# Kernel tuning notes

Hardware: AMD Instinct MI355X
Metric: run time of the kernel (lower is better)

Reference implementation:

```python
import jax, jax.numpy as jnp
import numpy as np

B, S, D, H = 16, 512, 1024, 16
DH = D // H  # 64


def setup_inputs() -> dict:
    key = jax.random.key(0)
    kx, kq, kk, kv = jax.random.split(key, 4)
    stdv = 1.0 / np.sqrt(DH)  # reset_param uses 1/sqrt(t.size(1)) = 1/sqrt(head_dim)
    x = jax.random.normal(kx, (B, S, D), dtype=jnp.float32)
    Wq = jax.random.uniform(kq, (H, D, DH), dtype=jnp.float32, minval=-stdv, maxval=stdv)
    Wk = jax.random.uniform(kk, (H, D, DH), dtype=jnp.float32, minval=-stdv, maxval=stdv)
    Wv = jax.random.uniform(kv, (H, D, DH), dtype=jnp.float32, minval=-stdv, maxval=stdv)
    return {"x": x, "Wq": Wq, "Wk": Wk, "Wv": Wv}


def reference(x, Wq, Wk, Wv):
    # x: [B, S, D]; Wq/Wk/Wv: [H, D, DH] (stacked per-head params)
    q = jnp.einsum('bsd,hde->bhse', x, Wq)  # [B,H,S,DH]
    k = jnp.einsum('bsd,hde->bhse', x, Wk)
    v = jnp.einsum('bsd,hde->bhse', x, Wv)
    # NOTE: original scales by sqrt(input_dim), not sqrt(head_dim)
    scale = 1.0 / jnp.sqrt(jnp.float32(D))
    scores = jnp.einsum('bhse,bhte->bhst', q, k) * scale  # [B,H,S,S]
    attn = jax.nn.softmax(scores, axis=-1)
    out = jnp.einsum('bhst,bhte->bhse', attn, v)  # [B,H,S,DH]
    # concat heads along feature dim (head order matches torch cat over loop)
    return out.transpose(0, 2, 1, 3).reshape(x.shape[0], x.shape[1], D)
```

## Files before the change

### kernel.cpp

```cpp
#include <hip/hip_runtime.h>
#include <math.h>

constexpr int B = 16, S = 512, D = 1024, H = 16, DH = 64;
constexpr int BH = B * H;

typedef short bf16x8 __attribute__((ext_vector_type(8)));
typedef float f32x4  __attribute__((ext_vector_type(4)));

__device__ __forceinline__ unsigned short f2bf(float f) {
    unsigned u = __float_as_uint(f);
    u += 0x7fff + ((u >> 16) & 1);
    return (unsigned short)(u >> 16);
}

#define VMC0  asm volatile("s_waitcnt vmcnt(0)" ::: "memory")
#define LGKM0 asm volatile("s_waitcnt lgkmcnt(0)" ::: "memory")
#define BARR  __builtin_amdgcn_s_barrier()

__global__ __launch_bounds__(256) void convert_all(
    const float* __restrict__ x, unsigned short* __restrict__ xb,
    const float* __restrict__ Wq, const float* __restrict__ Wk,
    const float* __restrict__ Wv, unsigned short* __restrict__ WbT)
{
    __shared__ float tile[64][65];
    const int t = threadIdx.x;
    const int bx = blockIdx.x;

    if (bx < 8192) {
        int i = bx * 256 + t;
        float4 v = ((const float4*)x)[i];
        ushort4 o;
        o.x = f2bf(v.x); o.y = f2bf(v.y); o.z = f2bf(v.z); o.w = f2bf(v.w);
        ((ushort4*)xb)[i] = o;
        return;
    }

    const int cw = bx - 8192;
    const int d0 = (cw & 15) * 64;
    const int h = (cw >> 4) & 15;
    const int m = cw >> 8;
    const float* W = ((m == 0) ? Wq : (m == 1) ? Wk : Wv) + (size_t)h * D * DH;
    {
        int e = t & 63, dr = t >> 6;
        #pragma unroll
        for (int i = 0; i < 16; ++i) {
            int d = dr * 16 + i;
            tile[d][e] = W[(size_t)(d0 + d) * DH + e];
        }
    }
    __syncthreads();
    {
        int d = t & 63, er = t >> 6;
        unsigned short* out = WbT + (size_t)(m * H + h) * DH * D;
        #pragma unroll
        for (int i = 0; i < 16; ++i) {
            int e = er * 16 + i;
            out[(size_t)e * D + d0 + d] = f2bf(tile[d][e]);
        }
    }
}

__device__ __forceinline__ void qkv_stage(
    const unsigned short* __restrict__ xb,
    const unsigned short* __restrict__ WbT,
    unsigned short* Ad, unsigned short* Bd,
    int r0, int n0, int k0, int w, int lrow8, int lg)
{
    #pragma unroll
    for (int i = 0; i < 4; ++i) {
        int c = w * 4 + i;
        int r = c * 8 + lrow8;
        int gg = lg ^ (r & 7);
        __builtin_amdgcn_global_load_lds(
            (const __attribute__((address_space(1))) void*)
                (xb + (size_t)(r0 + r) * D + k0 + gg * 8),
            (__attribute__((address_space(3))) void*)(Ad + c * 512),
            16, 0, 0);
        __builtin_amdgcn_global_load_lds(
            (const __attribute__((address_space(1))) void*)
                (WbT + (size_t)(n0 + r) * D + k0 + gg * 8),
            (__attribute__((address_space(3))) void*)(Bd + c * 512),
            16, 0, 0);
    }
}

__global__ __launch_bounds__(256) void qkv_gemm(
    const unsigned short* __restrict__ xb,
    const unsigned short* __restrict__ WbT,
    unsigned short* __restrict__ qkvb)
{
    __shared__ unsigned short As[2][128 * 64];
    __shared__ unsigned short Bs[2][128 * 64];

    const int t = threadIdx.x;
    const int w = t >> 6;
    const int wr = w >> 1, wc = w & 1;
    const int L = t & 63;
    const int lane15 = L & 15;
    const int quad = L >> 4;
    const int lrow8 = L >> 3;
    const int lg = L & 7;

    const int r0 = blockIdx.x * 128;
    const int n0 = blockIdx.y * 128;

    f32x4 acc[4][4] = {};

    qkv_stage(xb, WbT, &As[0][0], &Bs[0][0], r0, n0, 0, w, lrow8, lg);
    VMC0;
    BARR;

    #pragma unroll 2
    for (int kt = 0; kt < 16; ++kt) {
        const int cur = kt & 1;

        bf16x8 a[2][4], bb[2][4];
        #pragma unroll
        for (int ks = 0; ks < 2; ++ks) {
            int gk = ks * 4 + quad;
            #pragma unroll
            for (int rt = 0; rt < 4; ++rt) {
                int ml = wr * 64 + rt * 16 + lane15;
                a[ks][rt] = *(const bf16x8*)(&As[cur][0] + ml * 64 + ((gk ^ (ml & 7)) * 8));
            }
            #pragma unroll
            for (int ct = 0; ct < 4; ++ct) {
                int nl = wc * 64 + ct * 16 + lane15;
                bb[ks][ct] = *(const bf16x8*)(&Bs[cur][0] + nl * 64 + ((gk ^ (nl & 7)) * 8));
            }
        }
        __builtin_amdgcn_sched_barrier(0);

        if (kt < 15)
            qkv_stage(xb, WbT, &As[cur ^ 1][0], &Bs[cur ^ 1][0],
                      r0, n0, (kt + 1) * 64, w, lrow8, lg);

        __builtin_amdgcn_s_setprio(1);
        #pragma unroll
        for (int ks = 0; ks < 2; ++ks)
            #pragma unroll
            for (int rt = 0; rt < 4; ++rt)
                #pragma unroll
                for (int ct = 0; ct < 4; ++ct)
                    acc[rt][ct] = __builtin_amdgcn_mfma_f32_16x16x32_bf16(
                        a[ks][rt], bb[ks][ct], acc[rt][ct], 0, 0, 0);
        __builtin_amdgcn_s_setprio(0);

        VMC0;
        BARR;
    }

    const int m  = n0 >> 10;
    const int h  = ((n0 >> 6) + wc) & 15;
    const int bb_ = r0 >> 9;
    const int s0 = (r0 & 511) + wr * 64;

    if (m == 2) {
        unsigned short* outv = qkvb + ((size_t)(2 * BH) + (bb_ * H + h)) * (size_t)(S * DH);
        #pragma unroll
        for (int rt = 0; rt < 4; ++rt) {
            int srow = s0 + rt * 16 + quad * 4;
            #pragma unroll
            for (int ct = 0; ct < 4; ++ct) {
                int e = ct * 16 + lane15;
                ushort4 pk;
                pk.x = f2bf(acc[rt][ct][0]);
                pk.y = f2bf(acc[rt][ct][1]);
                pk.z = f2bf(acc[rt][ct][2]);
                pk.w = f2bf(acc[rt][ct][3]);
                *(ushort4*)(outv + (size_t)e * S + srow) = pk;
            }
        }
    } else {
        const float sc = (m == 0) ? 0.04508422002778011f : 1.0f;
        unsigned short* out = qkvb + ((size_t)m * BH + (bb_ * H + h)) * (size_t)(S * DH);
        #pragma unroll
        for (int rt = 0; rt < 4; ++rt) {
            #pragma unroll
            for (int ct = 0; ct < 4; ++ct) {
                int e = ct * 16 + lane15;
                #pragma unroll
                for (int r = 0; r < 4; ++r) {
                    int srow = s0 + rt * 16 + quad * 4 + r;
                    out[(size_t)srow * DH + e] = f2bf(acc[rt][ct][r] * sc);
                }
            }
        }
    }
}

__global__ __launch_bounds__(512, 4) void attn_mfma(
    const unsigned short* __restrict__ qkvb, float* __restrict__ out)
{
    __shared__ unsigned short KV[2][2][64 * 64];
    unsigned short* Qs = &KV[0][0][0];

    const int t = threadIdx.x;
    const int w = t >> 6;
    const int L = t & 63;
    const int lane15 = L & 15;
    const int quad = L >> 4;
    const int lrow8 = L >> 3;
    const int lg = L & 7;
    const int qr0 = blockIdx.x * 128;
    const int bh = blockIdx.y;
    const int b = bh >> 4, h = bh & 15;

    const unsigned short* qb = qkvb + (size_t)bh * S * DH;
    const unsigned short* kb = qkvb + (size_t)(BH + bh) * S * DH;
    const unsigned short* vt = qkvb + (size_t)(2 * BH + bh) * S * DH;

    #pragma unroll
    for (int p = 0; p < 2; ++p) {
        int base = p * 64 + w * 8;
        int r = base + lrow8;
        int gg = lg ^ (r & 7);
        __builtin_amdgcn_global_load_lds(
            (const __attribute__((address_space(1))) void*)
                (qb + (size_t)(qr0 + r) * DH + gg * 8),
            (__attribute__((address_space(3))) void*)(Qs + base * 64),
            16, 0, 0);
    }
    VMC0;
    BARR;

    bf16x8 qf[2];
    #pragma unroll
    for (int ks = 0; ks < 2; ++ks) {
        int ml = w * 16 + lane15;
        int gk = ks * 4 + quad;
        qf[ks] = *(const bf16x8*)(Qs + ml * 64 + ((gk ^ (lane15 & 7)) * 8));
    }
    LGKM0;
    BARR;

    {
        int r = w * 8 + lrow8;
        int gr = (r & 32) | ((r & 12) << 1) | ((r & 16) >> 2) | (r & 3);
        int gg = lg ^ (r & 7);
        __builtin_amdgcn_global_load_lds(
            (const __attribute__((address_space(1))) void*)
                (kb + (size_t)gr * DH + gg * 8),
            (__attribute__((address_space(3))) void*)(&KV[0][0][0] + (w * 8) * 64),
            16, 0, 0);
        __builtin_amdgcn_global_load_lds(
            (const __attribute__((address_space(1))) void*)
                (vt + (size_t)r * S + gg * 8),
            (__attribute__((address_space(3))) void*)(&KV[0][1][0] + (w * 8) * 64),
            16, 0, 0);
    }
    VMC0;
    BARR;

    f32x4 o[4] = {};
    float plsum = 0.f;

    #pragma unroll 2
    for (int kt = 0; kt < 8; ++kt) {
        const int cur = kt & 1;
        const unsigned short* Kt  = &KV[cur][0][0];
        const unsigned short* Vtl = &KV[cur][1][0];

        f32x4 st[4] = {};
        #pragma unroll
        for (int ks = 0; ks < 2; ++ks) {
            int gk = ks * 4 + quad;
            bf16x8 kf[4];
            #pragma unroll
            for (int ct = 0; ct < 4; ++ct) {
                int kr = ct * 16 + lane15;
                kf[ct] = *(const bf16x8*)(Kt + kr * 64 + ((gk ^ (lane15 & 7)) * 8));
            }
            __builtin_amdgcn_s_setprio(1);
            #pragma unroll
            for (int ct = 0; ct < 4; ++ct)
                st[ct] = __builtin_amdgcn_mfma_f32_16x16x32_bf16(
                    kf[ct], qf[ks], st[ct], 0, 0, 0);
            __builtin_amdgcn_s_setprio(0);
        }

        bf16x8 pB[2];
        {
            float rs = 0.f;
            union { unsigned u[4]; bf16x8 v; } pu[2];
            #pragma unroll
            for (int ct = 0; ct < 4; ++ct) {
                float p0 = exp2f(st[ct][0]);
                float p1 = exp2f(st[ct][1]);
                float p2 = exp2f(st[ct][2]);
                float p3 = exp2f(st[ct][3]);
                rs += (p0 + p1) + (p2 + p3);
                unsigned lo, hi;
                asm("v_cvt_pk_bf16_f32 %0, %1, %2" : "=v"(lo) : "v"(p0), "v"(p1));
                asm("v_cvt_pk_bf16_f32 %0, %1, %2" : "=v"(hi) : "v"(p2), "v"(p3));
                pu[ct >> 1].u[(ct & 1) * 2 + 0] = lo;
                pu[ct >> 1].u[(ct & 1) * 2 + 1] = hi;
            }
            pB[0] = pu[0].v;
            pB[1] = pu[1].v;
            plsum += rs;
        }

        #pragma unroll
        for (int ks = 0; ks < 2; ++ks) {
            int gk = ks * 4 + quad;
            bf16x8 vf[4];
            #pragma unroll
            for (int nt = 0; nt < 4; ++nt) {
                int dh = nt * 16 + lane15;
                vf[nt] = *(const bf16x8*)(Vtl + dh * 64 + ((gk ^ (lane15 & 7)) * 8));
            }
            __builtin_amdgcn_s_setprio(1);
            #pragma unroll
            for (int nt = 0; nt < 4; ++nt)
                o[nt] = __builtin_amdgcn_mfma_f32_16x16x32_bf16(
                    vf[nt], pB[ks], o[nt], 0, 0, 0);
            __builtin_amdgcn_s_setprio(0);
        }

        if (kt < 7) {
            int r = w * 8 + lrow8;
            int gr = (r & 32) | ((r & 12) << 1) | ((r & 16) >> 2) | (r & 3);
            int gg = lg ^ (r & 7);
            int kn = (kt + 1) * 64;
            __builtin_amdgcn_global_load_lds(
                (const __attribute__((address_space(1))) void*)
                    (kb + (size_t)(kn + gr) * DH + gg * 8),
                (__attribute__((address_space(3))) void*)(&KV[cur ^ 1][0][0] + (w * 8) * 64),
                16, 0, 0);
            __builtin_amdgcn_global_load_lds(
                (const __attribute__((address_space(1))) void*)
                    (vt + (size_t)r * S + kn + gg * 8),
                (__attribute__((address_space(3))) void*)(&KV[cur ^ 1][1][0] + (w * 8) * 64),
                16, 0, 0);
            VMC0;
            BARR;
        }
    }

    {
        float l = plsum;
        l += __shfl_xor(l, 16, 64);
        l += __shfl_xor(l, 32, 64);
        float inv = 1.0f / l;
        int srow = qr0 + w * 16 + lane15;
        float* op = out + (size_t)(b * S + srow) * D + h * DH;
        #pragma unroll
        for (int nt = 0; nt < 4; ++nt) {
            float4 v;
            v.x = o[nt][0] * inv;
            v.y = o[nt][1] * inv;
            v.z = o[nt][2] * inv;
            v.w = o[nt][3] * inv;
            *(float4*)(op + nt * 16 + quad * 4) = v;
        }
    }
}

extern "C" void kernel_launch(void* const* d_in, const int* in_sizes, int n_in,
                              void* d_out, int out_size, void* d_ws, size_t ws_size,
                              hipStream_t stream) {
    const float* x  = (const float*)d_in[0];
    const float* Wq = (const float*)d_in[1];
    const float* Wk = (const float*)d_in[2];
    const float* Wv = (const float*)d_in[3];
    float* outp = (float*)d_out;

    unsigned short* qkvb = (unsigned short*)d_ws;
    unsigned short* xb   = (unsigned short*)((char*)d_ws + 50331648);
    unsigned short* WbT  = (unsigned short*)((char*)d_ws + 67108864);

    convert_all<<<dim3(8192 + 768), 256, 0, stream>>>(x, xb, Wq, Wk, Wv, WbT);
    qkv_gemm<<<dim3(B * S / 128, 3 * H * DH / 128), 256, 0, stream>>>(xb, WbT, qkvb);
    attn_mfma<<<dim3(S / 128, BH), 512, 0, stream>>>(qkvb, outp);
}
```

Before: 180.4 us.

## Enlarge attention query tile per wave and prefetch K/V early

Each wave in the attention kernel now handles 64 query rows (4 MFMA row tiles) instead of 16, so each K/V fragment read from LDS is reused across four query tiles. Blocks shrink to 256 threads covering 256 query rows. All K and V fragments for a tile are read into registers up front, which lets the next tile's global-to-LDS prefetch start before the MFMA work instead of after it. The cost is much higher register pressure (score and output accumulators grow fourfold) and far fewer resident waves, which reduces latency hiding.

```diff
diff --git a/kernel.cpp b/kernel.cpp
--- a/kernel.cpp
+++ b/kernel.cpp
@@ -189,7 +189,30 @@
     }
 }
 
-__global__ __launch_bounds__(512, 4) void attn_mfma(
+__device__ __forceinline__ void stage_kv(
+    const unsigned short* __restrict__ kb, const unsigned short* __restrict__ vt,
+    int kt, unsigned short* Kd, unsigned short* Vd, int w, int lrow8, int lg)
+{
+    #pragma unroll
+    for (int i = 0; i < 2; ++i) {
+        int base = (w * 2 + i) * 8;
+        int r = base + lrow8;
+        int gr = (r & 32) | ((r & 12) << 1) | ((r & 16) >> 2) | (r & 3);
+        int gg = lg ^ (r & 7);
+        __builtin_amdgcn_global_load_lds(
+            (const __attribute__((address_space(1))) void*)
+                (kb + (size_t)(kt + gr) * DH + gg * 8),
+            (__attribute__((address_space(3))) void*)(Kd + base * 64),
+            16, 0, 0);
+        __builtin_amdgcn_global_load_lds(
+            (const __attribute__((address_space(1))) void*)
+                (vt + (size_t)r * S + kt + gg * 8),
+            (__attribute__((address_space(3))) void*)(Vd + base * 64),
+            16, 0, 0);
+    }
+}
+
+__global__ __launch_bounds__(256) void attn_mfma(
     const unsigned short* __restrict__ qkvb, float* __restrict__ out)
 {
     __shared__ unsigned short KV[2][2][64 * 64];
@@ -202,7 +225,7 @@
     const int quad = L >> 4;
     const int lrow8 = L >> 3;
     const int lg = L & 7;
-    const int qr0 = blockIdx.x * 128;
+    const int qr0 = blockIdx.x * 256;
     const int bh = blockIdx.y;
     const int b = bh >> 4, h = bh & 15;
 
@@ -211,8 +234,8 @@
     const unsigned short* vt = qkvb + (size_t)(2 * BH + bh) * S * DH;
 
     #pragma unroll
-    for (int p = 0; p < 2; ++p) {
-        int base = p * 64 + w * 8;
+    for (int i = 0; i < 8; ++i) {
+        int base = i * 32 + w * 8;
         int r = base + lrow8;
         int gg = lg ^ (r & 7);
         __builtin_amdgcn_global_load_lds(
@@ -224,71 +247,69 @@
     VMC0;
     BARR;
 
-    bf16x8 qf[2];
-    #pragma unroll
-    for (int ks = 0; ks < 2; ++ks) {
-        int ml = w * 16 + lane15;
-        int gk = ks * 4 + quad;
-        qf[ks] = *(const bf16x8*)(Qs + ml * 64 + ((gk ^ (lane15 & 7)) * 8));
-    }
+    bf16x8 qf[4][2];
+    #pragma unroll
+    for (int mt = 0; mt < 4; ++mt)
+        #pragma unroll
+        for (int ks = 0; ks < 2; ++ks) {
+            int ml = w * 64 + mt * 16 + lane15;
+            int gk = ks * 4 + quad;
+            qf[mt][ks] = *(const bf16x8*)(Qs + ml * 64 + ((gk ^ (lane15 & 7)) * 8));
+        }
     LGKM0;
     BARR;
 
-    {
-        int r = w * 8 + lrow8;
-        int gr = (r & 32) | ((r & 12) << 1) | ((r & 16) >> 2) | (r & 3);
-        int gg = lg ^ (r & 7);
-        __builtin_amdgcn_global_load_lds(
-            (const __attribute__((address_space(1))) void*)
-                (kb + (size_t)gr * DH + gg * 8),
-            (__attribute__((address_space(3))) void*)(&KV[0][0][0] + (w * 8) * 64),
-            16, 0, 0);
-        __builtin_amdgcn_global_load_lds(
-            (const __attribute__((address_space(1))) void*)
-                (vt + (size_t)r * S + gg * 8),
-            (__attribute__((address_space(3))) void*)(&KV[0][1][0] + (w * 8) * 64),
-            16, 0, 0);
-    }
+    stage_kv(kb, vt, 0, &KV[0][0][0], &KV[0][1][0], w, lrow8, lg);
     VMC0;
     BARR;
 
-    f32x4 o[4] = {};
-    float plsum = 0.f;
+    f32x4 o[4][4] = {};
+    float plsum[4] = {0.f, 0.f, 0.f, 0.f};
 
     #pragma unroll 2
     for (int kt = 0; kt < 8; ++kt) {
         const int cur = kt & 1;
-        const unsigned short* Kt  = &KV[cur][0][0];
-        const unsigned short* Vtl = &KV[cur][1][0];
-
-        f32x4 st[4] = {};
+
+        bf16x8 kf[2][4], vf[2][4];
         #pragma unroll
         for (int ks = 0; ks < 2; ++ks) {
             int gk = ks * 4 + quad;
-            bf16x8 kf[4];
             #pragma unroll
             for (int ct = 0; ct < 4; ++ct) {
                 int kr = ct * 16 + lane15;
-                kf[ct] = *(const bf16x8*)(Kt + kr * 64 + ((gk ^ (lane15 & 7)) * 8));
-            }
-            __builtin_amdgcn_s_setprio(1);
-            #pragma unroll
-            for (int ct = 0; ct < 4; ++ct)
-                st[ct] = __builtin_amdgcn_mfma_f32_16x16x32_bf16(
-                    kf[ct], qf[ks], st[ct], 0, 0, 0);
-            __builtin_amdgcn_s_setprio(0);
-        }
-
-        bf16x8 pB[2];
-        {
+                kf[ks][ct] = *(const bf16x8*)(&KV[cur][0][0] + kr * 64 + ((gk ^ (lane15 & 7)) * 8));
+                vf[ks][ct] = *(const bf16x8*)(&KV[cur][1][0] + kr * 64 + ((gk ^ (lane15 & 7)) * 8));
+            }
+        }
+        __builtin_amdgcn_sched_barrier(0);
+
+        if (kt < 7)
+            stage_kv(kb, vt, (kt + 1) * 64, &KV[cur ^ 1][0][0], &KV[cur ^ 1][1][0],
+                     w, lrow8, lg);
+
+        f32x4 st[4][4] = {};
+        __builtin_amdgcn_s_setprio(1);
+        #pragma unroll
+        for (int ks = 0; ks < 2; ++ks)
+            #pragma unroll
+            for (int mt = 0; mt < 4; ++mt)
+                #pragma unroll
+                for (int ct = 0; ct < 4; ++ct)
+                    st[mt][ct] = __builtin_amdgcn_mfma_f32_16x16x32_bf16(
+                        kf[ks][ct], qf[mt][ks], st[mt][ct], 0, 0, 0);
+        __builtin_amdgcn_s_setprio(0);
+
+        bf16x8 pB[4][2];
+        #pragma unroll
+        for (int mt = 0; mt < 4; ++mt) {
             float rs = 0.f;
             union { unsigned u[4]; bf16x8 v; } pu[2];
             #pragma unroll
             for (int ct = 0; ct < 4; ++ct) {
-                float p0 = exp2f(st[ct][0]);
-                float p1 = exp2f(st[ct][1]);
-                float p2 = exp2f(st[ct][2]);
-                float p3 = exp2f(st[ct][3]);
+                float p0 = exp2f(st[mt][ct][0]);
+                float p1 = exp2f(st[mt][ct][1]);
+                float p2 = exp2f(st[mt][ct][2]);
+                float p3 = exp2f(st[mt][ct][3]);
                 rs += (p0 + p1) + (p2 + p3);
                 unsigned lo, hi;
                 asm("v_cvt_pk_bf16_f32 %0, %1, %2" : "=v"(lo) : "v"(p0), "v"(p1));
@@ -296,62 +317,41 @@
                 pu[ct >> 1].u[(ct & 1) * 2 + 0] = lo;
                 pu[ct >> 1].u[(ct & 1) * 2 + 1] = hi;
             }
-            pB[0] = pu[0].v;
-            pB[1] = pu[1].v;
-            plsum += rs;
-        }
-
-        #pragma unroll
-        for (int ks = 0; ks < 2; ++ks) {
-            int gk = ks * 4 + quad;
-            bf16x8 vf[4];
-            #pragma unroll
-            for (int nt = 0; nt < 4; ++nt) {
-                int dh = nt * 16 + lane15;
-                vf[nt] = *(const bf16x8*)(Vtl + dh * 64 + ((gk ^ (lane15 & 7)) * 8));
-            }
-            __builtin_amdgcn_s_setprio(1);
-            #pragma unroll
-            for (int nt = 0; nt < 4; ++nt)
-                o[nt] = __builtin_amdgcn_mfma_f32_16x16x32_bf16(
-                    vf[nt], pB[ks], o[nt], 0, 0, 0);
-            __builtin_amdgcn_s_setprio(0);
-        }
-
-        if (kt < 7) {
-            int r = w * 8 + lrow8;
-            int gr = (r & 32) | ((r & 12) << 1) | ((r & 16) >> 2) | (r & 3);
-            int gg = lg ^ (r & 7);
-            int kn = (kt + 1) * 64;
-            __builtin_amdgcn_global_load_lds(
-                (const __attribute__((address_space(1))) void*)
-                    (kb + (size_t)(kn + gr) * DH + gg * 8),
-                (__attribute__((address_space(3))) void*)(&KV[cur ^ 1][0][0] + (w * 8) * 64),
-                16, 0, 0);
-            __builtin_amdgcn_global_load_lds(
-                (const __attribute__((address_space(1))) void*)
-                    (vt + (size_t)r * S + kn + gg * 8),
-                (__attribute__((address_space(3))) void*)(&KV[cur ^ 1][1][0] + (w * 8) * 64),
-                16, 0, 0);
-            VMC0;
-            BARR;
-        }
-    }
-
-    {
-        float l = plsum;
+            pB[mt][0] = pu[0].v;
+            pB[mt][1] = pu[1].v;
+            plsum[mt] += rs;
+        }
+
+        __builtin_amdgcn_s_setprio(1);
+        #pragma unroll
+        for (int ks = 0; ks < 2; ++ks)
+            #pragma unroll
+            for (int mt = 0; mt < 4; ++mt)
+                #pragma unroll
+                for (int nt = 0; nt < 4; ++nt)
+                    o[mt][nt] = __builtin_amdgcn_mfma_f32_16x16x32_bf16(
+                        vf[ks][nt], pB[mt][ks], o[mt][nt], 0, 0, 0);
+        __builtin_amdgcn_s_setprio(0);
+
+        VMC0;
+        BARR;
+    }
+
+    #pragma unroll
+    for (int mt = 0; mt < 4; ++mt) {
+        float l = plsum[mt];
         l += __shfl_xor(l, 16, 64);
         l += __shfl_xor(l, 32, 64);
         float inv = 1.0f / l;
-        int srow = qr0 + w * 16 + lane15;
+        int srow = qr0 + w * 64 + mt * 16 + lane15;
         float* op = out + (size_t)(b * S + srow) * D + h * DH;
         #pragma unroll
         for (int nt = 0; nt < 4; ++nt) {
             float4 v;
-            v.x = o[nt][0] * inv;
-            v.y = o[nt][1] * inv;
-            v.z = o[nt][2] * inv;
-            v.w = o[nt][3] * inv;
+            v.x = o[mt][nt][0] * inv;
+            v.y = o[mt][nt][1] * inv;
+            v.z = o[mt][nt][2] * inv;
+            v.w = o[mt][nt][3] * inv;
             *(float4*)(op + nt * 16 + quad * 4) = v;
         }
     }
@@ -372,5 +372,5 @@
 
     convert_all<<<dim3(8192 + 768), 256, 0, stream>>>(x, xb, Wq, Wk, Wv, WbT);
     qkv_gemm<<<dim3(B * S / 128, 3 * H * DH / 128), 256, 0, stream>>>(xb, WbT, qkvb);
-    attn_mfma<<<dim3(S / 128, BH), 512, 0, stream>>>(qkvb, outp);
-}
+    attn_mfma<<<dim3(S / 256, BH), 256, 0, stream>>>(qkvb, outp);
+}
```

After: 189.0 us. 1.05x slower.
